# Optimization experiments

Hardware: AMD Instinct MI355X
Metric: run time of the kernel (lower is better)

Reference implementation:

```python
import jax, jax.numpy as jnp
import numpy as np

EMB = 1024
HEADS = 16
DK = EMB // HEADS

def setup_inputs() -> dict:
    key = jax.random.key(0)
    ks = jax.random.split(key, 5)
    scale = 0.02
    return {
        "x": jax.random.normal(ks[0], (4, 2048, EMB), dtype=jnp.float32),
        "W_in": jax.random.normal(ks[1], (3 * EMB, EMB), dtype=jnp.float32) * scale,
        "b_in": jax.random.normal(ks[2], (3 * EMB,), dtype=jnp.float32) * scale,
        "W_out": jax.random.normal(ks[3], (EMB, EMB), dtype=jnp.float32) * scale,
        "b_out": jax.random.normal(ks[4], (EMB,), dtype=jnp.float32) * scale,
    }

def reference(x, W_in, b_in, W_out, b_out):
    B, T, C = x.shape
    qkv = x @ W_in.T + b_in                      # [B,T,3C]
    q, k, v = jnp.split(qkv, 3, axis=-1)
    def heads(t):
        return t.reshape(B, T, HEADS, DK).transpose(0, 2, 1, 3)  # [B,H,T,Dk]
    q, k, v = heads(q), heads(k), heads(v)
    scores = jnp.einsum("bhqd,bhkd->bhqk", q, k) / jnp.sqrt(jnp.float32(DK))
    causal = jnp.tril(jnp.ones((T, T), dtype=bool))
    scores = jnp.where(causal, scores, jnp.finfo(scores.dtype).min)
    attn = jax.nn.softmax(scores, axis=-1)
    y = jnp.einsum("bhqk,bhkd->bhqd", attn, v)   # [B,H,T,Dk]
    y = y.transpose(0, 2, 1, 3).reshape(B, T, C)
    return y @ W_out.T + b_out
```

## Files before the change

### kernel.cpp

```cpp
#include <hip/hip_runtime.h>
#include <hip/hip_bf16.h>

#define EMB   1024
#define HEADS 16
#define DKV   64
#define BB    4
#define TT    2048
#define MTOT  8192

#define QSCALE 0.1803368801111204f
#define RESCALE_THR 8.0f

typedef short bf16x8 __attribute__((ext_vector_type(8)));
typedef float f32x4  __attribute__((ext_vector_type(4)));

__device__ __forceinline__ ushort bf16_bits(float f) {
    union { __hip_bfloat16 h; ushort u; } cv;
    cv.h = __float2bfloat16(f);
    return cv.u;
}
__device__ __forceinline__ unsigned pack_bf16(float lo, float hi) {
    return (unsigned)bf16_bits(lo) | ((unsigned)bf16_bits(hi) << 16);
}
__device__ __forceinline__ void gload16(const void* g, void* lds) {
    __builtin_amdgcn_global_load_lds(
        (const __attribute__((address_space(1))) unsigned*)g,
        (__attribute__((address_space(3))) unsigned*)lds, 16, 0, 0);
}
__device__ __forceinline__ int swz128(int row, int bytecol) {
    return row * 128 + (bytecol ^ ((row & 7) << 4));
}

__global__ void cvt_all(const float* __restrict__ x,   ushort* __restrict__ xo,
                        const float* __restrict__ wi,  ushort* __restrict__ wio,
                        const float* __restrict__ wo,  ushort* __restrict__ woo) {
    const int n4x = (MTOT * EMB) / 4;
    const int n4i = (3 * EMB * EMB) / 4;
    const int n4o = (EMB * EMB) / 4;
    int idx = blockIdx.x * blockDim.x + threadIdx.x;
    int stride = gridDim.x * blockDim.x;
    for (int i = idx; i < n4x + n4i + n4o; i += stride) {
        const float* in;
        ushort* out;
        int j = i;
        if (j < n4x)            { in = x;  out = xo;  }
        else if (j < n4x + n4i) { in = wi; out = wio; j -= n4x; }
        else                    { in = wo; out = woo; j -= n4x + n4i; }
        float4 v = reinterpret_cast<const float4*>(in)[j];
        ushort4 o;
        o.x = bf16_bits(v.x);
        o.y = bf16_bits(v.y);
        o.z = bf16_bits(v.z);
        o.w = bf16_bits(v.w);
        reinterpret_cast<ushort4*>(out)[j] = o;
    }
}

template<int EPI>
__global__ __launch_bounds__(256) void gemm_bt(
    const ushort* __restrict__ Ab, const ushort* __restrict__ Wb,
    const float* __restrict__ bias,
    ushort* __restrict__ qo, ushort* __restrict__ ko, ushort* __restrict__ vo,
    float* __restrict__ outf,
    int Msz, int Nsz, int Ksz)
{
    __shared__ __align__(16) ushort Sh[4][128 * 32];

    int tid = threadIdx.x;
    int mtiles = Msz >> 7;
    int bm = blockIdx.x % mtiles;
    int bn = blockIdx.x / mtiles;
    int m0 = bm << 7, n0 = bn << 7;
    int w = tid >> 6, l = tid & 63;
    int wr = w >> 1, wc = w & 1;
    int lr = l & 15, lk = (l >> 4) << 3;
    int srow = w * 16 + (l >> 2);
    int scol = (l & 3) << 3;

    f32x4 acc[4][4] = {};

    auto STAGE = [&](int buf, int k0) {
        #pragma unroll
        for (int p = 0; p < 2; ++p) {
            int row = p * 64 + srow;
            gload16(&Ab[(size_t)(m0 + row) * Ksz + k0 + scol],
                    (char*)Sh[buf * 2]     + (size_t)(p * 256 + w * 64) * 16);
            gload16(&Wb[(size_t)(n0 + row) * Ksz + k0 + scol],
                    (char*)Sh[buf * 2 + 1] + (size_t)(p * 256 + w * 64) * 16);
        }
    };

    STAGE(0, 0);
    int buf = 0;
    for (int k0 = 0; k0 < Ksz; k0 += 32) {
        __syncthreads();
        if (k0 + 32 < Ksz) STAGE(buf ^ 1, k0 + 32);
        const ushort* As = Sh[buf * 2];
        const ushort* Bs = Sh[buf * 2 + 1];

        bf16x8 a[4], b[4];
        #pragma unroll
        for (int mi = 0; mi < 4; ++mi)
            a[mi] = *(const bf16x8*)(&As[(wr * 64 + mi * 16 + lr) * 32 + lk]);
        #pragma unroll
        for (int ni = 0; ni < 4; ++ni)
            b[ni] = *(const bf16x8*)(&Bs[(wc * 64 + ni * 16 + lr) * 32 + lk]);
        __builtin_amdgcn_s_setprio(1);
        #pragma unroll
        for (int mi = 0; mi < 4; ++mi)
            #pragma unroll
            for (int ni = 0; ni < 4; ++ni)
                acc[mi][ni] = __builtin_amdgcn_mfma_f32_16x16x32_bf16(
                    a[mi], b[ni], acc[mi][ni], 0, 0, 0);
        __builtin_amdgcn_s_setprio(0);
        buf ^= 1;
    }

    if (EPI == 1) {
        #pragma unroll
        for (int mi = 0; mi < 4; ++mi)
            #pragma unroll
            for (int ni = 0; ni < 4; ++ni) {
                int n = n0 + wc * 64 + ni * 16 + lr;
                float bv = bias[n];
                #pragma unroll
                for (int r = 0; r < 4; ++r) {
                    int m = m0 + wr * 64 + mi * 16 + ((l >> 4) << 2) + r;
                    outf[(size_t)m * Nsz + n] = acc[mi][ni][r] + bv;
                }
            }
    } else {
        int which = n0 >> 10;
        if (which < 2) {
            ushort* dst = (which == 0) ? qo : ko;
            float qs = (which == 0) ? QSCALE : 1.f;
            #pragma unroll
            for (int mi = 0; mi < 4; ++mi)
                #pragma unroll
                for (int ni = 0; ni < 4; ++ni) {
                    int n = n0 + wc * 64 + ni * 16 + lr;
                    float bv = bias[n];
                    int rem = n & 1023;
                    int hd = rem >> 6, dk = rem & 63;
                    #pragma unroll
                    for (int r = 0; r < 4; ++r) {
                        int m = m0 + wr * 64 + mi * 16 + ((l >> 4) << 2) + r;
                        int b_ = m >> 11, t_ = m & 2047;
                        dst[((((size_t)b_ * HEADS + hd) * TT + t_) << 6) + dk] =
                            bf16_bits((acc[mi][ni][r] + bv) * qs);
                    }
                }
        } else {
            char* Tb = (char*)Sh;
            int b_ = m0 >> 11;
            int row_r = tid >> 1;
            int rem = (n0 + row_r) & 1023;
            int hd = rem >> 6, dk = rem & 63;
            size_t vrow = ((size_t)(b_ * HEADS + hd) * DKV + dk) * TT;
            int tbase = (m0 & 2047) + (tid & 1) * 32;
            #pragma unroll
            for (int h = 0; h < 2; ++h) {
                __syncthreads();
                if (wr == h) {
                    #pragma unroll
                    for (int ni = 0; ni < 4; ++ni) {
                        int n_l = wc * 64 + ni * 16 + lr;
                        float bv = bias[n0 + n_l];
                        #pragma unroll
                        for (int mi = 0; mi < 4; ++mi) {
                            uint2 u;
                            u.x = pack_bf16(acc[mi][ni][0] + bv, acc[mi][ni][1] + bv);
                            u.y = pack_bf16(acc[mi][ni][2] + bv, acc[mi][ni][3] + bv);
                            *(uint2*)(Tb + swz128(n_l, mi * 32 + ((l >> 4) << 3))) = u;
                        }
                    }
                }
                __syncthreads();
                #pragma unroll
                for (int qq = 0; qq < 4; ++qq) {
                    int4 d = *(const int4*)(Tb + swz128(row_r, (tid & 1) * 64 + qq * 16));
                    *(int4*)(&vo[vrow + tbase + h * 64 + qq * 8]) = d;
                }
            }
        }
    }
}

__device__ __forceinline__ void strip_tile(
    const char* __restrict__ Kbuf, const char* __restrict__ Vbuf, char* __restrict__ Plw,
    bf16x8 q0, bf16x8 q1,
    float& m_run, float& l_run, f32x4 (&o)[4],
    int lr, int g, bool diag, int qloc)
{
    f32x4 st[4];
    #pragma unroll
    for (int kt = 0; kt < 4; ++kt) {
        bf16x8 a0 = *(const bf16x8*)(Kbuf + swz128(kt * 16 + lr, g * 16));
        bf16x8 a1 = *(const bf16x8*)(Kbuf + swz128(kt * 16 + lr, 64 + g * 16));
        f32x4 z = {};
        __builtin_amdgcn_s_setprio(1);
        z = __builtin_amdgcn_mfma_f32_16x16x32_bf16(a0, q0, z, 0, 0, 0);
        z = __builtin_amdgcn_mfma_f32_16x16x32_bf16(a1, q1, z, 0, 0, 0);
        __builtin_amdgcn_s_setprio(0);
        st[kt] = z;
    }
    if (diag) {
        #pragma unroll
        for (int kt = 0; kt < 4; ++kt)
            #pragma unroll
            for (int r = 0; r < 4; ++r) {
                int kvloc = kt * 16 + g * 4 + r;
                st[kt][r] = (kvloc <= qloc) ? st[kt][r] : -1e30f;
            }
    }
    float mx = -1e30f;
    #pragma unroll
    for (int kt = 0; kt < 4; ++kt)
        #pragma unroll
        for (int r = 0; r < 4; ++r) mx = fmaxf(mx, st[kt][r]);
    mx = fmaxf(mx, __shfl_xor(mx, 16));
    mx = fmaxf(mx, __shfl_xor(mx, 32));

    if (!__all(mx - m_run <= RESCALE_THR)) {
        float mnew = fmaxf(m_run, mx);
        float alpha = exp2f(m_run - mnew);
        m_run = mnew;
        l_run *= alpha;
        float al0 = __shfl(alpha, g * 4 + 0);
        float al1 = __shfl(alpha, g * 4 + 1);
        float al2 = __shfl(alpha, g * 4 + 2);
        float al3 = __shfl(alpha, g * 4 + 3);
        #pragma unroll
        for (int dt = 0; dt < 4; ++dt) {
            o[dt][0] *= al0; o[dt][1] *= al1; o[dt][2] *= al2; o[dt][3] *= al3;
        }
    }

    float rs = 0.f;
    #pragma unroll
    for (int kt = 0; kt < 4; ++kt) {
        float p0 = exp2f(st[kt][0] - m_run);
        float p1 = exp2f(st[kt][1] - m_run);
        float p2 = exp2f(st[kt][2] - m_run);
        float p3 = exp2f(st[kt][3] - m_run);
        rs += (p0 + p1) + (p2 + p3);
        uint2 u;
        u.x = pack_bf16(p0, p1);
        u.y = pack_bf16(p2, p3);
        *(uint2*)(Plw + swz128(lr, kt * 32 + g * 8)) = u;
    }
    rs += __shfl_xor(rs, 16);
    rs += __shfl_xor(rs, 32);
    l_run += rs;

    bf16x8 pa0 = *(const bf16x8*)(Plw + swz128(lr, g * 16));
    bf16x8 pa1 = *(const bf16x8*)(Plw + swz128(lr, 64 + g * 16));

    __builtin_amdgcn_s_setprio(1);
    #pragma unroll
    for (int dt = 0; dt < 4; ++dt) {
        bf16x8 b0 = *(const bf16x8*)(Vbuf + swz128(dt * 16 + lr, g * 16));
        bf16x8 b1 = *(const bf16x8*)(Vbuf + swz128(dt * 16 + lr, 64 + g * 16));
        o[dt] = __builtin_amdgcn_mfma_f32_16x16x32_bf16(pa0, b0, o[dt], 0, 0, 0);
        o[dt] = __builtin_amdgcn_mfma_f32_16x16x32_bf16(pa1, b1, o[dt], 0, 0, 0);
    }
    __builtin_amdgcn_s_setprio(0);
}

__global__ __launch_bounds__(256, 3) void attn_kernel(
    const ushort* __restrict__ qb, const ushort* __restrict__ kb,
    const ushort* __restrict__ vtb, ushort* __restrict__ yb)
{
    __shared__ __align__(16) char Ks[2][64 * 128];
    __shared__ __align__(16) char Vs[2][64 * 128];
    __shared__ __align__(16) char Pl[4][16 * 128];

    int tid = threadIdx.x;
    int w = tid >> 6, l = tid & 63;
    int bid = blockIdx.x;
    int swz = (bid & 7) * 128 + (bid >> 3);
    int pair = swz & 15;
    int bh = swz >> 4;
    int qtA = 31 - pair, qtB = pair;

    const ushort* Q  = qb  + (size_t)bh * TT * DKV;
    const ushort* K  = kb  + (size_t)bh * TT * DKV;
    const ushort* Vt = vtb + (size_t)bh * DKV * TT;
    int lr = l & 15, g = l >> 4;
    int qA0 = qtA * 64 + w * 16;
    int qB0 = qtB * 64 + w * 16;

    bf16x8 qaA0 = *(const bf16x8*)(&Q[(size_t)(qA0 + lr) * DKV + g * 8]);
    bf16x8 qaA1 = *(const bf16x8*)(&Q[(size_t)(qA0 + lr) * DKV + 32 + g * 8]);
    bf16x8 qaB0 = *(const bf16x8*)(&Q[(size_t)(qB0 + lr) * DKV + g * 8]);
    bf16x8 qaB1 = *(const bf16x8*)(&Q[(size_t)(qB0 + lr) * DKV + 32 + g * 8]);

    int srow = w * 8 + (l >> 3);
    int scel = ((((l & 7) * 16) ^ ((l >> 3) << 4)) >> 1);

    float mA = -1e30f, lA = 0.f, mB = -1e30f, lB = 0.f;
    f32x4 oA[4] = {}, oB[4] = {};
    int nt = qtA + 1;

    #pragma unroll
    for (int p = 0; p < 2; ++p) {
        int row = p * 32 + srow;
        gload16(&K [(size_t)row * DKV + scel], (char*)Ks[0] + (size_t)(p * 256 + w * 64) * 16);
        gload16(&Vt[(size_t)row * TT  + scel], (char*)Vs[0] + (size_t)(p * 256 + w * 64) * 16);
    }

    for (int jt = 0; jt < nt; ++jt) {
        int buf = jt & 1;
        __syncthreads();

        if (jt + 1 < nt) {
            int kv1 = (jt + 1) * 64;
            #pragma unroll
            for (int p = 0; p < 2; ++p) {
                int row = p * 32 + srow;
                gload16(&K [(size_t)(kv1 + row) * DKV + scel],
                        (char*)Ks[buf ^ 1] + (size_t)(p * 256 + w * 64) * 16);
                gload16(&Vt[(size_t)row * TT + kv1 + scel],
                        (char*)Vs[buf ^ 1] + (size_t)(p * 256 + w * 64) * 16);
            }
        }

        strip_tile(Ks[buf], Vs[buf], Pl[w], qaA0, qaA1, mA, lA, oA,
                   lr, g, jt == qtA, w * 16 + lr);
        if (jt <= qtB)
            strip_tile(Ks[buf], Vs[buf], Pl[w], qaB0, qaB1, mB, lB, oB,
                       lr, g, jt == qtB, w * 16 + lr);
    }

    int b_ = bh >> 4, h_ = bh & 15;
    {
        float li0 = 1.f / __shfl(lA, g * 4 + 0);
        float li1 = 1.f / __shfl(lA, g * 4 + 1);
        float li2 = 1.f / __shfl(lA, g * 4 + 2);
        float li3 = 1.f / __shfl(lA, g * 4 + 3);
        #pragma unroll
        for (int dt = 0; dt < 4; ++dt) {
            int d_ = h_ * 64 + dt * 16 + lr;
            size_t base = ((size_t)b_ * TT + (qA0 + g * 4)) * EMB + d_;
            yb[base]           = bf16_bits(oA[dt][0] * li0);
            yb[base + EMB]     = bf16_bits(oA[dt][1] * li1);
            yb[base + 2 * EMB] = bf16_bits(oA[dt][2] * li2);
            yb[base + 3 * EMB] = bf16_bits(oA[dt][3] * li3);
        }
    }
    {
        float li0 = 1.f / __shfl(lB, g * 4 + 0);
        float li1 = 1.f / __shfl(lB, g * 4 + 1);
        float li2 = 1.f / __shfl(lB, g * 4 + 2);
        float li3 = 1.f / __shfl(lB, g * 4 + 3);
        #pragma unroll
        for (int dt = 0; dt < 4; ++dt) {
            int d_ = h_ * 64 + dt * 16 + lr;
            size_t base = ((size_t)b_ * TT + (qB0 + g * 4)) * EMB + d_;
            yb[base]           = bf16_bits(oB[dt][0] * li0);
            yb[base + EMB]     = bf16_bits(oB[dt][1] * li1);
            yb[base + 2 * EMB] = bf16_bits(oB[dt][2] * li2);
            yb[base + 3 * EMB] = bf16_bits(oB[dt][3] * li3);
        }
    }
}

extern "C" void kernel_launch(void* const* d_in, const int* in_sizes, int n_in,
                              void* d_out, int out_size, void* d_ws, size_t ws_size,
                              hipStream_t stream) {
    const float* x     = (const float*)d_in[0];
    const float* W_in  = (const float*)d_in[1];
    const float* b_in  = (const float*)d_in[2];
    const float* W_out = (const float*)d_in[3];
    const float* b_out = (const float*)d_in[4];
    float* out = (float*)d_out;
    char* ws = (char*)d_ws;

    ushort* xb  = (ushort*)(ws);
    ushort* wib = (ushort*)(ws + 16777216);
    ushort* wob = (ushort*)(ws + 23068672);
    ushort* qbp = (ushort*)(ws + 25165824);
    ushort* kbp = (ushort*)(ws + 41943040);
    ushort* vbp = (ushort*)(ws + 58720256);
    ushort* ybp = (ushort*)(ws + 75497472);

    cvt_all<<<1280, 256, 0, stream>>>(x, xb, W_in, wib, W_out, wob);

    gemm_bt<0><<<dim3((MTOT / 128) * (3 * EMB / 128)), dim3(256), 0, stream>>>(
        xb, wib, b_in, qbp, kbp, vbp, nullptr, MTOT, 3 * EMB, EMB);

    attn_kernel<<<dim3(BB * HEADS * 16), dim3(256), 0, stream>>>(
        qbp, kbp, vbp, ybp);

    gemm_bt<1><<<dim3((MTOT / 128) * (EMB / 128)), dim3(256), 0, stream>>>(
        ybp, wob, b_out, nullptr, nullptr, nullptr, out, MTOT, EMB, EMB);
}
```

Baseline: 185.8 us.

## Process four query strips per attention block to raise K/V tile reuse

Each attention block now handles two 128-row query supertiles, balanced as a high and low pair, with four 16-row strips per wave instead of two. Every K/V tile loaded into shared memory therefore feeds up to four strip computations, which halves K/V global traffic and barrier count per unit of work. The grid is halved to 512 blocks, so there are fewer waves to fill 256 CUs, and register pressure rises from the extra Q fragments and accumulators, which may hurt occupancy under launch_bounds(256,3).

Result: slower. 194.8 us (+4.9%).

```diff
diff --git a/kernel.cpp b/kernel.cpp
--- a/kernel.cpp
+++ b/kernel.cpp
@@ -267,6 +267,25 @@
     __builtin_amdgcn_s_setprio(0);
 }
 
+__device__ __forceinline__ void write_o(
+    ushort* __restrict__ yb, int b_, int h_, int q0, int g, int lr,
+    float l_run, f32x4 (&o)[4])
+{
+    float li0 = 1.f / __shfl(l_run, g * 4 + 0);
+    float li1 = 1.f / __shfl(l_run, g * 4 + 1);
+    float li2 = 1.f / __shfl(l_run, g * 4 + 2);
+    float li3 = 1.f / __shfl(l_run, g * 4 + 3);
+    #pragma unroll
+    for (int dt = 0; dt < 4; ++dt) {
+        int d_ = h_ * 64 + dt * 16 + lr;
+        size_t base = ((size_t)b_ * TT + (q0 + g * 4)) * EMB + d_;
+        yb[base]           = bf16_bits(o[dt][0] * li0);
+        yb[base + EMB]     = bf16_bits(o[dt][1] * li1);
+        yb[base + 2 * EMB] = bf16_bits(o[dt][2] * li2);
+        yb[base + 3 * EMB] = bf16_bits(o[dt][3] * li3);
+    }
+}
+
 __global__ __launch_bounds__(256, 3) void attn_kernel(
     const ushort* __restrict__ qb, const ushort* __restrict__ kb,
     const ushort* __restrict__ vtb, ushort* __restrict__ yb)
@@ -278,29 +297,35 @@
     int tid = threadIdx.x;
     int w = tid >> 6, l = tid & 63;
     int bid = blockIdx.x;
-    int swz = (bid & 7) * 128 + (bid >> 3);
-    int pair = swz & 15;
-    int bh = swz >> 4;
-    int qtA = 31 - pair, qtB = pair;
+    int swz = (bid & 7) * 64 + (bid >> 3);
+    int pair = swz & 7;
+    int bh = swz >> 3;
+    int sA = 15 - pair, sB = pair;
 
     const ushort* Q  = qb  + (size_t)bh * TT * DKV;
     const ushort* K  = kb  + (size_t)bh * TT * DKV;
     const ushort* Vt = vtb + (size_t)bh * DKV * TT;
     int lr = l & 15, g = l >> 4;
-    int qA0 = qtA * 64 + w * 16;
-    int qB0 = qtB * 64 + w * 16;
-
-    bf16x8 qaA0 = *(const bf16x8*)(&Q[(size_t)(qA0 + lr) * DKV + g * 8]);
-    bf16x8 qaA1 = *(const bf16x8*)(&Q[(size_t)(qA0 + lr) * DKV + 32 + g * 8]);
-    bf16x8 qaB0 = *(const bf16x8*)(&Q[(size_t)(qB0 + lr) * DKV + g * 8]);
-    bf16x8 qaB1 = *(const bf16x8*)(&Q[(size_t)(qB0 + lr) * DKV + 32 + g * 8]);
+    int qA = sA * 128 + w * 16;
+    int qB = sB * 128 + w * 16;
+
+    bf16x8 qaA0_0 = *(const bf16x8*)(&Q[(size_t)(qA + lr) * DKV + g * 8]);
+    bf16x8 qaA0_1 = *(const bf16x8*)(&Q[(size_t)(qA + lr) * DKV + 32 + g * 8]);
+    bf16x8 qaA1_0 = *(const bf16x8*)(&Q[(size_t)(qA + 64 + lr) * DKV + g * 8]);
+    bf16x8 qaA1_1 = *(const bf16x8*)(&Q[(size_t)(qA + 64 + lr) * DKV + 32 + g * 8]);
+    bf16x8 qaB0_0 = *(const bf16x8*)(&Q[(size_t)(qB + lr) * DKV + g * 8]);
+    bf16x8 qaB0_1 = *(const bf16x8*)(&Q[(size_t)(qB + lr) * DKV + 32 + g * 8]);
+    bf16x8 qaB1_0 = *(const bf16x8*)(&Q[(size_t)(qB + 64 + lr) * DKV + g * 8]);
+    bf16x8 qaB1_1 = *(const bf16x8*)(&Q[(size_t)(qB + 64 + lr) * DKV + 32 + g * 8]);
 
     int srow = w * 8 + (l >> 3);
     int scel = ((((l & 7) * 16) ^ ((l >> 3) << 4)) >> 1);
 
-    float mA = -1e30f, lA = 0.f, mB = -1e30f, lB = 0.f;
-    f32x4 oA[4] = {}, oB[4] = {};
-    int nt = qtA + 1;
+    float mA0 = -1e30f, lA0 = 0.f, mA1 = -1e30f, lA1 = 0.f;
+    float mB0 = -1e30f, lB0 = 0.f, mB1 = -1e30f, lB1 = 0.f;
+    f32x4 oA0[4] = {}, oA1[4] = {}, oB0[4] = {}, oB1[4] = {};
+    int dA = 2 * sA, dB = 2 * sB;
+    int nt = dA + 2;
 
     #pragma unroll
     for (int p = 0; p < 2; ++p) {
@@ -309,6 +334,7 @@
         gload16(&Vt[(size_t)row * TT  + scel], (char*)Vs[0] + (size_t)(p * 256 + w * 64) * 16);
     }
 
+    int qloc = w * 16 + lr;
     for (int jt = 0; jt < nt; ++jt) {
         int buf = jt & 1;
         __syncthreads();
@@ -325,44 +351,24 @@
             }
         }
 
-        strip_tile(Ks[buf], Vs[buf], Pl[w], qaA0, qaA1, mA, lA, oA,
-                   lr, g, jt == qtA, w * 16 + lr);
-        if (jt <= qtB)
-            strip_tile(Ks[buf], Vs[buf], Pl[w], qaB0, qaB1, mB, lB, oB,
-                       lr, g, jt == qtB, w * 16 + lr);
+        strip_tile(Ks[buf], Vs[buf], Pl[w], qaA1_0, qaA1_1, mA1, lA1, oA1,
+                   lr, g, jt == dA + 1, qloc);
+        if (jt <= dA)
+            strip_tile(Ks[buf], Vs[buf], Pl[w], qaA0_0, qaA0_1, mA0, lA0, oA0,
+                       lr, g, jt == dA, qloc);
+        if (jt <= dB + 1)
+            strip_tile(Ks[buf], Vs[buf], Pl[w], qaB1_0, qaB1_1, mB1, lB1, oB1,
+                       lr, g, jt == dB + 1, qloc);
+        if (jt <= dB)
+            strip_tile(Ks[buf], Vs[buf], Pl[w], qaB0_0, qaB0_1, mB0, lB0, oB0,
+                       lr, g, jt == dB, qloc);
     }
 
     int b_ = bh >> 4, h_ = bh & 15;
-    {
-        float li0 = 1.f / __shfl(lA, g * 4 + 0);
-        float li1 = 1.f / __shfl(lA, g * 4 + 1);
-        float li2 = 1.f / __shfl(lA, g * 4 + 2);
-        float li3 = 1.f / __shfl(lA, g * 4 + 3);
-        #pragma unroll
-        for (int dt = 0; dt < 4; ++dt) {
-            int d_ = h_ * 64 + dt * 16 + lr;
-            size_t base = ((size_t)b_ * TT + (qA0 + g * 4)) * EMB + d_;
-            yb[base]           = bf16_bits(oA[dt][0] * li0);
-            yb[base + EMB]     = bf16_bits(oA[dt][1] * li1);
-            yb[base + 2 * EMB] = bf16_bits(oA[dt][2] * li2);
-            yb[base + 3 * EMB] = bf16_bits(oA[dt][3] * li3);
-        }
-    }
-    {
-        float li0 = 1.f / __shfl(lB, g * 4 + 0);
-        float li1 = 1.f / __shfl(lB, g * 4 + 1);
-        float li2 = 1.f / __shfl(lB, g * 4 + 2);
-        float li3 = 1.f / __shfl(lB, g * 4 + 3);
-        #pragma unroll
-        for (int dt = 0; dt < 4; ++dt) {
-            int d_ = h_ * 64 + dt * 16 + lr;
-            size_t base = ((size_t)b_ * TT + (qB0 + g * 4)) * EMB + d_;
-            yb[base]           = bf16_bits(oB[dt][0] * li0);
-            yb[base + EMB]     = bf16_bits(oB[dt][1] * li1);
-            yb[base + 2 * EMB] = bf16_bits(oB[dt][2] * li2);
-            yb[base + 3 * EMB] = bf16_bits(oB[dt][3] * li3);
-        }
-    }
+    write_o(yb, b_, h_, qA,      g, lr, lA0, oA0);
+    write_o(yb, b_, h_, qA + 64, g, lr, lA1, oA1);
+    write_o(yb, b_, h_, qB,      g, lr, lB0, oB0);
+    write_o(yb, b_, h_, qB + 64, g, lr, lB1, oB1);
 }
 
 extern "C" void kernel_launch(void* const* d_in, const int* in_sizes, int n_in,
@@ -389,7 +395,7 @@
     gemm_bt<0><<<dim3((MTOT / 128) * (3 * EMB / 128)), dim3(256), 0, stream>>>(
         xb, wib, b_in, qbp, kbp, vbp, nullptr, MTOT, 3 * EMB, EMB);
 
-    attn_kernel<<<dim3(BB * HEADS * 16), dim3(256), 0, stream>>>(
+    attn_kernel<<<dim3(BB * HEADS * 8), dim3(256), 0, stream>>>(
         qbp, kbp, vbp, ybp);
 
     gemm_bt<1><<<dim3((MTOT / 128) * (EMB / 128)), dim3(256), 0, stream>>>(
```
